# Performance work log

Measured on AMD Instinct MI355X. Metric: run time of the kernel, lower is better.

The kernel has to match this reference:

```python
import jax, jax.numpy as jnp
import numpy as np

D_MODEL = 1024
NHEAD = 16
HEAD_DIM = D_MODEL // NHEAD
DIM_FF = 4096
B, TC, TP = 4, 1024, 1024
EPS = 1e-5


def _layernorm(x, g, b):
    mu = jnp.mean(x, axis=-1, keepdims=True)
    var = jnp.mean(jnp.square(x - mu), axis=-1, keepdims=True)
    return (x - mu) * jax.lax.rsqrt(var + EPS) * g + b


def setup_inputs() -> dict:
    key = jax.random.key(0)
    ks = jax.random.split(key, 12)
    s = 0.02
    return {
        "x": jax.random.normal(ks[0], (B, TC, D_MODEL), jnp.float32),
        "Kp": jax.random.normal(ks[1], (B, NHEAD, TP, HEAD_DIM), jnp.float32),
        "Vp": jax.random.normal(ks[2], (B, NHEAD, TP, HEAD_DIM), jnp.float32),
        "pos_offset": TP,
        "wqkv": jax.random.normal(ks[3], (D_MODEL, 3 * D_MODEL), jnp.float32) * s,
        "bqkv": jnp.zeros((3 * D_MODEL,), jnp.float32),
        "wo": jax.random.normal(ks[4], (D_MODEL, D_MODEL), jnp.float32) * s,
        "bo": jnp.zeros((D_MODEL,), jnp.float32),
        "g1": jnp.ones((D_MODEL,), jnp.float32),
        "be1": jnp.zeros((D_MODEL,), jnp.float32),
        "g2": jnp.ones((D_MODEL,), jnp.float32),
        "be2": jnp.zeros((D_MODEL,), jnp.float32),
        "w1": jax.random.normal(ks[5], (D_MODEL, DIM_FF), jnp.float32) * s,
        "bf1": jnp.zeros((DIM_FF,), jnp.float32),
        "w2": jax.random.normal(ks[6], (DIM_FF, D_MODEL), jnp.float32) * s,
        "bf2": jnp.zeros((D_MODEL,), jnp.float32),
    }


def reference(x, Kp, Vp, pos_offset, wqkv, bqkv, wo, bo, g1, be1, g2, be2, w1, bf1, w2, bf2):
    Bsz, Tc, D = x.shape
    H, Dh = NHEAD, HEAD_DIM
    h = _layernorm(x, g1, be1)
    qkv = (h @ wqkv + bqkv).reshape(Bsz, Tc, 3, H, Dh).transpose(2, 0, 3, 1, 4)
    q, k_new, v_new = qkv[0], qkv[1], qkv[2]  # [B,H,Tc,Dh]
    K = jnp.concatenate([Kp, k_new], axis=2)  # [B,H,Tk,Dh]
    V = jnp.concatenate([Vp, v_new], axis=2)
    Tk = K.shape[2]
    scale = Dh ** -0.5
    # fused causal-masked attention; equivalent to the per-token loop:
    # query i attends keys j with j <= pos_offset + i
    scores = jnp.einsum("bhqd,bhkd->bhqk", q, K) * scale
    q_idx = jnp.arange(Tc)[:, None]
    k_idx = jnp.arange(Tk)[None, :]
    mask = k_idx <= (pos_offset + q_idx)  # [Tc,Tk]
    scores = jnp.where(mask, scores, jnp.finfo(scores.dtype).min)
    attn = jax.nn.softmax(scores, axis=-1)
    o = jnp.einsum("bhqk,bhkd->bhqd", attn, V)
    o = o.transpose(0, 2, 1, 3).reshape(Bsz, Tc, D)
    x = x + o @ wo + bo
    h2 = _layernorm(x, g2, be2)
    ff = jax.nn.gelu(h2 @ w1 + bf1, approximate=False) @ w2 + bf2
    x = x + ff
    return x, K, V
```

## Files before the change

### kernel.cpp

```cpp
#include <hip/hip_runtime.h>
#include <math.h>

#define DM   1024
#define NH   16
#define DH   64
#define DFF  4096
#define BSZ  4
#define TCC  1024
#define TPP  1024
#define TKK  2048
#define NTOK (BSZ*TCC)

typedef __attribute__((ext_vector_type(8))) short bf16x8;
typedef __attribute__((ext_vector_type(4))) float f32x4;

__device__ __forceinline__ unsigned short f2bf(float x) {
  union { float f; unsigned u; } v; v.f = x;
  unsigned r = v.u + 0x7fffu + ((v.u >> 16) & 1u);
  return (unsigned short)(r >> 16);
}
__device__ __forceinline__ unsigned pk2(float a, float b) {
  return (unsigned)f2bf(a) | ((unsigned)f2bf(b) << 16);
}

__device__ __forceinline__ void gload16(const void* g, void* l) {
  __builtin_amdgcn_global_load_lds(
      (const __attribute__((address_space(1))) void*)g,
      (__attribute__((address_space(3))) void*)l, 16, 0, 0);
}

__device__ __forceinline__ float wave_reduce_sum(float v) {
#pragma unroll
  for (int off = 32; off > 0; off >>= 1)
    v += __shfl_down(v, off, 64);
  return v;
}

__device__ __forceinline__ float gelu_f(float x) {
  float z = fabsf(x) * 0.70710678118654752440f;
  float t = 1.0f / (1.0f + 0.3275911f * z);
  float y = t * (0.254829592f +
            t * (-0.284496736f +
            t * (1.421413741f +
            t * (-1.453152027f +
            t * 1.061405429f))));
  float e = __expf(-z * z);
  float erfz = 1.0f - y * e;
  float s = (x >= 0.0f) ? erfz : -erfz;
  return 0.5f * x * (1.0f + s);
}

__global__ __launch_bounds__(256) void castT_kernel(
    const float* __restrict__ W, unsigned short* __restrict__ Wt, int K, int N) {
  __shared__ float tile[32][33];
  int nb = blockIdx.x << 5, kb = blockIdx.y << 5;
  int c = threadIdx.x & 31, r8 = threadIdx.x >> 5;
#pragma unroll
  for (int i = 0; i < 32; i += 8)
    tile[r8 + i][c] = W[(size_t)(kb + r8 + i) * N + nb + c];
  __syncthreads();
#pragma unroll
  for (int i = 0; i < 32; i += 8)
    Wt[(size_t)(nb + r8 + i) * K + kb + c] = f2bf(tile[c][r8 + i]);
}

__global__ __launch_bounds__(256) void castVt_kernel(
    const float* __restrict__ V, unsigned short* __restrict__ Vt) {
  __shared__ float tile[32][33];
  int z = blockIdx.z;
  const float* W = V + (size_t)z * TKK * DH;
  unsigned short* Wt = Vt + (size_t)z * DH * TKK;
  int nb = blockIdx.x << 5;
  int kb = blockIdx.y << 5;
  int c = threadIdx.x & 31, r8 = threadIdx.x >> 5;
#pragma unroll
  for (int i = 0; i < 32; i += 8)
    tile[r8 + i][c] = W[(size_t)(kb + r8 + i) * DH + nb + c];
  __syncthreads();
#pragma unroll
  for (int i = 0; i < 32; i += 8)
    Wt[(size_t)(nb + r8 + i) * TKK + kb + c] = f2bf(tile[c][r8 + i]);
}

__global__ __launch_bounds__(256) void copy_kv_kernel(
    const float4* __restrict__ Kp, const float4* __restrict__ Vp,
    float4* __restrict__ Kout, float4* __restrict__ Vout,
    unsigned short* __restrict__ Kbf) {
  int idx = blockIdx.x * 256 + threadIdx.x;
  int r = idx >> 4;
  int c = idx & 15;
  int dr = (r >> 10) * TKK + (r & 1023);
  float4 kv = Kp[idx];
  Kout[dr * 16 + c] = kv;
  Vout[dr * 16 + c] = Vp[idx];
  if (Kbf != nullptr) {
    uint2 pk;
    pk.x = pk2(kv.x, kv.y);
    pk.y = pk2(kv.z, kv.w);
    *(uint2*)(Kbf + (size_t)(dr * 16 + c) * 4) = pk;
  }
}

__global__ __launch_bounds__(256) void ln_kernel(
    const float* __restrict__ x, const float* __restrict__ g,
    const float* __restrict__ b, unsigned short* __restrict__ out) {
  __shared__ float red[8];
  int row = blockIdx.x;
  int tid = threadIdx.x;
  const float4* xr = (const float4*)(x + (size_t)row * DM);
  float4 xv = xr[tid];
  float s  = xv.x + xv.y + xv.z + xv.w;
  float ss = xv.x*xv.x + xv.y*xv.y + xv.z*xv.z + xv.w*xv.w;
  s  = wave_reduce_sum(s);
  ss = wave_reduce_sum(ss);
  int lane = tid & 63, wid = tid >> 6;
  if (lane == 0) { red[wid] = s; red[4 + wid] = ss; }
  __syncthreads();
  s  = red[0] + red[1] + red[2] + red[3];
  ss = red[4] + red[5] + red[6] + red[7];
  float mu  = s * (1.0f / DM);
  float var = ss * (1.0f / DM) - mu * mu;
  float rs  = rsqrtf(var + 1e-5f);
  float4 gv = ((const float4*)g)[tid];
  float4 bv = ((const float4*)b)[tid];
  ushort4 ov;
  ov.x = f2bf((xv.x - mu) * rs * gv.x + bv.x);
  ov.y = f2bf((xv.y - mu) * rs * gv.y + bv.y);
  ov.z = f2bf((xv.z - mu) * rs * gv.z + bv.z);
  ov.w = f2bf((xv.w - mu) * rs * gv.w + bv.w);
  *(ushort4*)&out[(size_t)row * DM + tid * 4] = ov;
}

template <int MODE, int NSPLIT>
__global__ __launch_bounds__(512) void mm8_kernel(
    const unsigned short* __restrict__ A, const unsigned short* __restrict__ Bt,
    const float* __restrict__ bias, const float* __restrict__ res,
    float* __restrict__ outf, unsigned short* __restrict__ outb,
    float* __restrict__ Kc, float* __restrict__ Vc,
    unsigned short* __restrict__ Kbfp,
    int M, int N, int K) {
  __shared__ __align__(16) short lds[4][2][8192];
  int tid = threadIdx.x;
  int l = tid & 63, w = tid >> 6;
  int wr = w >> 2, wc = w & 3;
  int cidx = l & 15, rg = l >> 4;
  int m0 = blockIdx.y << 8, n0 = blockIdx.x << 8;
  int z = (NSPLIT > 1) ? blockIdx.z : 0;
  int KS = K / NSPLIT;

  int r0 = tid >> 2;
  int cb = (((tid & 3) ^ ((r0 >> 1) & 3)) << 4);
  const char* gA = (const char*)A + (size_t)(m0 + r0) * 2 * K + cb + (size_t)2 * z * KS;
  const char* gB = (const char*)Bt + (size_t)(n0 + r0) * 2 * K + cb + (size_t)2 * z * KS;
  size_t rskip = (size_t)128 * 2 * K;

  int xcs = ((rg ^ ((cidx >> 1) & 3)) << 4);
  int offA = (wr * 128 + cidx) * 64 + xcs;
  int offB = (wc * 64 + cidx) * 64 + xcs;

  f32x4 acc[8][4] = {};
  int NT = KS >> 5;

  auto stage = [&](int t, int half) {
    char* la = (char*)&lds[t & 3][0][0] + tid * 16 + half * 8192;
    char* lb = (char*)&lds[t & 3][1][0] + tid * 16 + half * 8192;
    const char* sa = gA + t * 64 + (half ? rskip : 0);
    const char* sb = gB + t * 64 + (half ? rskip : 0);
    gload16(sa, la);
    gload16(sb, lb);
  };

  stage(0, 0); stage(0, 1);
  stage(1, 0); stage(1, 1);
  stage(2, 0); stage(2, 1);
  asm volatile("s_waitcnt vmcnt(8)" ::: "memory");
  __builtin_amdgcn_sched_barrier(0);
  __builtin_amdgcn_s_barrier();

  for (int t = 0; t < NT; ++t) {
    const char* pa = (const char*)&lds[t & 3][0][0];
    const char* pb = (const char*)&lds[t & 3][1][0];
    bf16x8 af[4], bg[4], a2[4];
#pragma unroll
    for (int i = 0; i < 4; ++i)
      af[i] = *(const bf16x8*)(pa + offA + i * 1024);
#pragma unroll
    for (int j = 0; j < 4; ++j)
      bg[j] = *(const bf16x8*)(pb + offB + j * 1024);
    if (t + 3 < NT) stage(t + 3, 0);
    __builtin_amdgcn_s_barrier();
    asm volatile("s_waitcnt lgkmcnt(0)" ::: "memory");
    __builtin_amdgcn_sched_barrier(0);
    __builtin_amdgcn_s_setprio(1);
#pragma unroll
    for (int i = 0; i < 4; ++i)
#pragma unroll
      for (int j = 0; j < 4; ++j)
        acc[i][j] = __builtin_amdgcn_mfma_f32_16x16x32_bf16(
            af[i], bg[j], acc[i][j], 0, 0, 0);
    __builtin_amdgcn_s_setprio(0);
    __builtin_amdgcn_s_barrier();
#pragma unroll
    for (int i = 0; i < 4; ++i)
      a2[i] = *(const bf16x8*)(pa + offA + (i + 4) * 1024);
    if (t + 3 < NT) stage(t + 3, 1);
    if (t + 3 < NT) {
      asm volatile("s_waitcnt vmcnt(8)" ::: "memory");
    } else if (t + 2 < NT) {
      asm volatile("s_waitcnt vmcnt(4)" ::: "memory");
    } else {
      asm volatile("s_waitcnt vmcnt(0)" ::: "memory");
    }
    __builtin_amdgcn_sched_barrier(0);
    __builtin_amdgcn_s_barrier();
    asm volatile("s_waitcnt lgkmcnt(0)" ::: "memory");
    __builtin_amdgcn_sched_barrier(0);
    __builtin_amdgcn_s_setprio(1);
#pragma unroll
    for (int i = 0; i < 4; ++i)
#pragma unroll
      for (int j = 0; j < 4; ++j)
        acc[i + 4][j] = __builtin_amdgcn_mfma_f32_16x16x32_bf16(
            a2[i], bg[j], acc[i + 4][j], 0, 0, 0);
    __builtin_amdgcn_s_setprio(0);
    __builtin_amdgcn_s_barrier();
  }

#pragma unroll
  for (int i = 0; i < 8; ++i) {
#pragma unroll
    for (int j = 0; j < 4; ++j) {
      int col = n0 + wc * 64 + j * 16 + cidx;
      float bb = bias[col];
#pragma unroll
      for (int r = 0; r < 4; ++r) {
        int row = m0 + wr * 128 + i * 16 + rg * 4 + r;
        float v = acc[i][j][r] + bb;
        if (MODE == 0) {
          int which = col >> 10, c = col & 1023;
          int hh = c >> 6, dd = c & 63;
          int b = row >> 10, tt = row & 1023;
          size_t base = (size_t)(b * NH + hh);
          if (which == 0)      outb[(base * TCC + tt) * DH + dd] = f2bf(v * 0.125f);
          else if (which == 1) {
            size_t off = (base * TKK + TPP + tt) * DH + dd;
            Kc[off] = v;
            if (Kbfp != nullptr) Kbfp[off] = f2bf(v);
          } else               Vc[(base * TKK + TPP + tt) * DH + dd] = v;
        } else if (MODE == 2) {
          outb[(size_t)row * N + col] = f2bf(gelu_f(v));
        } else {
          size_t off = (size_t)row * N + col;
          float add = acc[i][j][r];
          if (z == 0) add += bb + res[off];
          unsafeAtomicAdd(&outf[off], add);
        }
      }
    }
  }
}

template <int MODE, int DEPTH>
__global__ __launch_bounds__(256) void mm_kernel(
    const unsigned short* __restrict__ A, const unsigned short* __restrict__ Bt,
    const float* __restrict__ bias, const float* __restrict__ res,
    float* __restrict__ outf, unsigned short* __restrict__ outb,
    int M, int N, int K) {
  __shared__ __align__(16) short As[DEPTH * 128 * 32];
  __shared__ __align__(16) short Bs[DEPTH * 128 * 32];
  int tid = threadIdx.x;
  int w = tid >> 6, l = tid & 63;
  int m0 = blockIdx.y << 7, n0 = blockIdx.x << 7;
  int wm = (w >> 1) << 6, wn = (w & 1) << 6;
  int cidx = l & 15, rg = l >> 4;
  f32x4 acc[4][4] = {};

  int idx0 = w * 1024 + l * 16;
  int idx1 = idx0 + 4096;
  const char* gA0 = (const char*)A + (size_t)(m0 + (idx0 >> 6)) * 2 * K + (idx0 & 63);
  const char* gA1 = (const char*)A + (size_t)(m0 + (idx1 >> 6)) * 2 * K + (idx1 & 63);
  const char* gB0 = (const char*)Bt + (size_t)(n0 + (idx0 >> 6)) * 2 * K + (idx0 & 63);
  const char* gB1 = (const char*)Bt + (size_t)(n0 + (idx1 >> 6)) * 2 * K + (idx1 & 63);

  auto stage = [&](int bsel) {
    char* base_a = (char*)As + bsel * 8192;
    char* base_b = (char*)Bs + bsel * 8192;
    gload16(gA0, base_a + idx0); gload16(gA1, base_a + idx1);
    gload16(gB0, base_b + idx0); gload16(gB1, base_b + idx1);
    gA0 += 64; gA1 += 64; gB0 += 64; gB1 += 64;
  };
  auto compute = [&](int bsel) {
    const short* pa = As + bsel * 4096;
    const short* pb = Bs + bsel * 4096;
    bf16x8 af[4], bfr[4];
#pragma unroll
    for (int i = 0; i < 4; ++i) {
      af[i]  = *(const bf16x8*)&pa[(wm + i * 16 + cidx) * 32 + rg * 8];
      bfr[i] = *(const bf16x8*)&pb[(wn + i * 16 + cidx) * 32 + rg * 8];
    }
#pragma unroll
    for (int i = 0; i < 4; ++i)
#pragma unroll
      for (int j = 0; j < 4; ++j)
        acc[i][j] = __builtin_amdgcn_mfma_f32_16x16x32_bf16(
            af[i], bfr[j], acc[i][j], 0, 0, 0);
  };

  int nt = K >> 5;
  stage(0); stage(1); stage(2);
  for (int t = 0; t < nt - 3; ++t) {
    asm volatile("s_waitcnt vmcnt(8)" ::: "memory");
    __builtin_amdgcn_sched_barrier(0);
    __builtin_amdgcn_s_barrier();
    __builtin_amdgcn_sched_barrier(0);
    stage((t + 3) & 3);
    compute(t & 3);
  }
  asm volatile("s_waitcnt vmcnt(8)" ::: "memory");
  __builtin_amdgcn_sched_barrier(0);
  __builtin_amdgcn_s_barrier();
  __builtin_amdgcn_sched_barrier(0);
  compute((nt - 3) & 3);
  asm volatile("s_waitcnt vmcnt(4)" ::: "memory");
  __builtin_amdgcn_sched_barrier(0);
  __builtin_amdgcn_s_barrier();
  __builtin_amdgcn_sched_barrier(0);
  compute((nt - 2) & 3);
  asm volatile("s_waitcnt vmcnt(0)" ::: "memory");
  __builtin_amdgcn_sched_barrier(0);
  __builtin_amdgcn_s_barrier();
  __builtin_amdgcn_sched_barrier(0);
  compute((nt - 1) & 3);

#pragma unroll
  for (int i = 0; i < 4; ++i) {
#pragma unroll
    for (int j = 0; j < 4; ++j) {
      int col = n0 + wn + j * 16 + cidx;
      float bb = bias[col];
#pragma unroll
      for (int r = 0; r < 4; ++r) {
        int row = m0 + wm + i * 16 + rg * 4 + r;
        float v = acc[i][j][r] + bb;
        size_t off = (size_t)row * N + col;
        outf[off] = res[off] + v;
      }
    }
  }
}

template <int KBF>
__global__ __launch_bounds__(256) void attn_kernel(
    const unsigned short* __restrict__ Qb, const float* __restrict__ K,
    const unsigned short* __restrict__ Kb16,
    const unsigned short* __restrict__ Vtb, const int* __restrict__ posp,
    unsigned short* __restrict__ o) {
  __shared__ __align__(16) unsigned short Qs[64][72];
  __shared__ __align__(16) unsigned short Ks[64][72];
  __shared__ __align__(16) unsigned short Vts[64][72];
  __shared__ __align__(16) unsigned short Pw[4][16][72];
  int tid = threadIdx.x;
  int w = tid >> 6, lane = tid & 63;
  int l15 = lane & 15, quad = lane >> 4;
  int blk = blockIdx.x;
  int bh = blk >> 4;
  int qbase = (blk & 15) << 6;
  int b = bh >> 4, h = bh & 15;
  int pos = *posp;

  {
    int r = tid >> 2, cg = (tid & 3) << 4;
    const unsigned short* src = Qb + ((size_t)bh * TCC + qbase + r) * DH + cg;
    *(uint4*)&Qs[r][cg]     = *(const uint4*)src;
    *(uint4*)&Qs[r][cg + 8] = *(const uint4*)(src + 8);
  }
  __syncthreads();
  bf16x8 aq0 = *(const bf16x8*)&Qs[16 * w + l15][quad * 8];
  bf16x8 aq1 = *(const bf16x8*)&Qs[16 * w + l15][32 + quad * 8];

  f32x4 accO[4] = {};
  f32x4 accL = {};
  bf16x8 ones;
#pragma unroll
  for (int i = 0; i < 8; ++i) ones[i] = (short)0x3F80;

  int nk = pos + qbase + 64; if (nk > TKK) nk = TKK;
  int ntiles = nk >> 6;
  const float* Kbh = K + (size_t)bh * TKK * DH;
  const unsigned short* Kbh16 = Kb16 + (size_t)bh * TKK * DH;
  const unsigned short* Vbh = Vtb + (size_t)bh * DH * TKK;

  for (int t = 0; t < ntiles; ++t) {
    int kt = t << 6;
    {
      int r = tid >> 2, cg = (tid & 3) << 4;
      if (KBF) {
        const unsigned short* ks = Kbh16 + (size_t)(kt + r) * DH + cg;
        *(uint4*)&Ks[r][cg]     = *(const uint4*)ks;
        *(uint4*)&Ks[r][cg + 8] = *(const uint4*)(ks + 8);
      } else {
        const float* ks = Kbh + (size_t)(kt + r) * DH + cg;
        float4 k0 = *(const float4*)ks,       k1 = *(const float4*)(ks + 4);
        float4 k2 = *(const float4*)(ks + 8), k3 = *(const float4*)(ks + 12);
        uint4 p0, p1;
        p0.x = pk2(k0.x, k0.y); p0.y = pk2(k0.z, k0.w);
        p0.z = pk2(k1.x, k1.y); p0.w = pk2(k1.z, k1.w);
        p1.x = pk2(k2.x, k2.y); p1.y = pk2(k2.z, k2.w);
        p1.z = pk2(k3.x, k3.y); p1.w = pk2(k3.z, k3.w);
        *(uint4*)&Ks[r][cg]     = p0;
        *(uint4*)&Ks[r][cg + 8] = p1;
      }
      const unsigned short* vs = Vbh + (size_t)r * TKK + kt + cg;
      *(uint4*)&Vts[r][cg]     = *(const uint4*)vs;
      *(uint4*)&Vts[r][cg + 8] = *(const uint4*)(vs + 8);
    }
    __syncthreads();
    f32x4 accS[4] = {};
    __builtin_amdgcn_s_setprio(1);
#pragma unroll
    for (int j = 0; j < 4; ++j) {
      bf16x8 bk0 = *(const bf16x8*)&Ks[16 * j + l15][quad * 8];
      bf16x8 bk1 = *(const bf16x8*)&Ks[16 * j + l15][32 + quad * 8];
      accS[j] = __builtin_amdgcn_mfma_f32_16x16x32_bf16(aq0, bk0, accS[j], 0, 0, 0);
      accS[j] = __builtin_amdgcn_mfma_f32_16x16x32_bf16(aq1, bk1, accS[j], 0, 0, 0);
    }
    __builtin_amdgcn_s_setprio(0);
    bool edge = (kt + 63 > pos + qbase);
#pragma unroll
    for (int j = 0; j < 4; ++j) {
      int key = kt + 16 * j + l15;
#pragma unroll
      for (int r = 0; r < 4; ++r) {
        float p = __expf(accS[j][r]);
        if (edge && key > pos + qbase + 16 * w + quad * 4 + r) p = 0.f;
        Pw[w][quad * 4 + r][16 * j + l15] = f2bf(p);
      }
    }
    bf16x8 ap0 = *(const bf16x8*)&Pw[w][l15][quad * 8];
    bf16x8 ap1 = *(const bf16x8*)&Pw[w][l15][32 + quad * 8];
    __builtin_amdgcn_s_setprio(1);
    accL = __builtin_amdgcn_mfma_f32_16x16x32_bf16(ap0, ones, accL, 0, 0, 0);
    accL = __builtin_amdgcn_mfma_f32_16x16x32_bf16(ap1, ones, accL, 0, 0, 0);
#pragma unroll
    for (int j2 = 0; j2 < 4; ++j2) {
      bf16x8 bv0 = *(const bf16x8*)&Vts[16 * j2 + l15][quad * 8];
      bf16x8 bv1 = *(const bf16x8*)&Vts[16 * j2 + l15][32 + quad * 8];
      accO[j2] = __builtin_amdgcn_mfma_f32_16x16x32_bf16(ap0, bv0, accO[j2], 0, 0, 0);
      accO[j2] = __builtin_amdgcn_mfma_f32_16x16x32_bf16(ap1, bv1, accO[j2], 0, 0, 0);
    }
    __builtin_amdgcn_s_setprio(0);
    __syncthreads();
  }
#pragma unroll
  for (int r = 0; r < 4; ++r) {
    float inv = 1.0f / accL[r];
    int qg = qbase + 16 * w + quad * 4 + r;
    size_t base = (((size_t)(b * TCC + qg)) * NH + h) * DH;
#pragma unroll
    for (int j2 = 0; j2 < 4; ++j2)
      o[base + 16 * j2 + l15] = f2bf(accO[j2][r] * inv);
  }
}

extern "C" void kernel_launch(void* const* d_in, const int* in_sizes, int n_in,
                              void* d_out, int out_size, void* d_ws, size_t ws_size,
                              hipStream_t stream) {
  (void)in_sizes; (void)n_in; (void)out_size;
  const float* x    = (const float*)d_in[0];
  const float* Kp   = (const float*)d_in[1];
  const float* Vp   = (const float*)d_in[2];
  const int*   posp = (const int*)d_in[3];
  const float* wqkv = (const float*)d_in[4];
  const float* bqkv = (const float*)d_in[5];
  const float* wo   = (const float*)d_in[6];
  const float* bo   = (const float*)d_in[7];
  const float* g1   = (const float*)d_in[8];
  const float* be1  = (const float*)d_in[9];
  const float* g2   = (const float*)d_in[10];
  const float* be2  = (const float*)d_in[11];
  const float* w1   = (const float*)d_in[12];
  const float* bf1  = (const float*)d_in[13];
  const float* w2   = (const float*)d_in[14];
  const float* bf2  = (const float*)d_in[15];

  float* xout = (float*)d_out;
  float* Kout = xout + (size_t)BSZ * TCC * DM;
  float* Vout = Kout + (size_t)BSZ * NH * TKK * DH;

  const size_t MB = 1024 * 1024;
  char* ws = (char*)d_ws;
  unsigned short* wqkvT = (unsigned short*)(ws);
  unsigned short* woT   = (unsigned short*)(ws + 6 * MB);
  unsigned short* w1T   = (unsigned short*)(ws + 8 * MB);
  unsigned short* w2T   = (unsigned short*)(ws + 16 * MB);
  unsigned short* hbf   = (unsigned short*)(ws + 24 * MB);
  unsigned short* ffbf  = (unsigned short*)(ws + 32 * MB);
  unsigned short* Qbuf  = (unsigned short*)(ws + 32 * MB);
  unsigned short* obf   = (unsigned short*)(ws + 40 * MB);
  unsigned short* Vtb   = (unsigned short*)(ws + 48 * MB);
  unsigned short* Kbf   = (ws_size >= 80 * MB)
                            ? (unsigned short*)(ws + 64 * MB) : nullptr;
  bool big = (ws_size >= 96 * MB);
  float* x2 = big ? (float*)(ws + 80 * MB) : xout;

  if (big) {
    hipMemsetAsync(x2,   0, (size_t)NTOK * DM * sizeof(float), stream);
    hipMemsetAsync(xout, 0, (size_t)NTOK * DM * sizeof(float), stream);
  }

  castT_kernel<<<dim3(96, 32),  dim3(256), 0, stream>>>(wqkv, wqkvT, DM, 3 * DM);
  castT_kernel<<<dim3(32, 32),  dim3(256), 0, stream>>>(wo,   woT,   DM, DM);
  castT_kernel<<<dim3(128, 32), dim3(256), 0, stream>>>(w1,   w1T,   DM, DFF);
  castT_kernel<<<dim3(32, 128), dim3(256), 0, stream>>>(w2,   w2T,   DFF, DM);

  copy_kv_kernel<<<dim3(4096), dim3(256), 0, stream>>>(
      (const float4*)Kp, (const float4*)Vp, (float4*)Kout, (float4*)Vout, Kbf);
  ln_kernel<<<dim3(NTOK), dim3(256), 0, stream>>>(x, g1, be1, hbf);
  mm8_kernel<0, 1><<<dim3(12, 16), dim3(512), 0, stream>>>(
      hbf, wqkvT, bqkv, nullptr, nullptr, Qbuf, Kout, Vout, Kbf, NTOK, 3 * DM, DM);
  castVt_kernel<<<dim3(2, 64, 64), dim3(256), 0, stream>>>(Vout, Vtb);
  if (Kbf != nullptr)
    attn_kernel<1><<<dim3(1024), dim3(256), 0, stream>>>(Qbuf, Kout, Kbf, Vtb, posp, obf);
  else
    attn_kernel<0><<<dim3(1024), dim3(256), 0, stream>>>(Qbuf, Kout, Kbf, Vtb, posp, obf);

  if (big) {
    mm8_kernel<3, 4><<<dim3(4, 16, 4), dim3(512), 0, stream>>>(
        obf, woT, bo, x, x2, nullptr, nullptr, nullptr, nullptr, NTOK, DM, DM);
    ln_kernel<<<dim3(NTOK), dim3(256), 0, stream>>>(x2, g2, be2, hbf);
    mm8_kernel<2, 1><<<dim3(16, 16), dim3(512), 0, stream>>>(
        hbf, w1T, bf1, nullptr, nullptr, ffbf, nullptr, nullptr, nullptr, NTOK, DFF, DM);
    mm8_kernel<3, 4><<<dim3(4, 16, 4), dim3(512), 0, stream>>>(
        ffbf, w2T, bf2, x2, xout, nullptr, nullptr, nullptr, nullptr, NTOK, DM, DFF);
  } else {
    mm_kernel<1, 4><<<dim3(8, 32), dim3(256), 0, stream>>>(
        obf, woT, bo, x, x2, nullptr, NTOK, DM, DM);
    ln_kernel<<<dim3(NTOK), dim3(256), 0, stream>>>(x2, g2, be2, hbf);
    mm8_kernel<2, 1><<<dim3(16, 16), dim3(512), 0, stream>>>(
        hbf, w1T, bf1, nullptr, nullptr, ffbf, nullptr, nullptr, nullptr, NTOK, DFF, DM);
    mm_kernel<1, 4><<<dim3(8, 32), dim3(256), 0, stream>>>(
        ffbf, w2T, bf2, x2, xout, nullptr, NTOK, DM, DFF);
  }
}
```

Measured before the change: 584.1 us.

## Replace atomic split-K output projections with plain partial stores plus reduction kernel

The out-projection now always uses the non-split mm_kernel, so its atomic split-K path and the two memsets are gone. The FF2 GEMM uses a 2-way split-K that writes plain stores into two workspace partial buffers, and a new elementwise kernel adds both partials, the bias and the residual into the output. This removes atomic contention and the zero-fill traffic, at the cost of an extra launch and a read/write pass over two 16MB partial buffers. pfA aliases the transposed-weight region at ws offset 0 and pfB aliases the Kbf region, which reuses buffers that are no longer needed at that point.

```diff
diff --git a/kernel.cpp b/kernel.cpp
--- a/kernel.cpp
+++ b/kernel.cpp
@@ -131,6 +131,21 @@
   *(ushort4*)&out[(size_t)row * DM + tid * 4] = ov;
 }
 
+__global__ __launch_bounds__(256) void reduce2_kernel(
+    float* __restrict__ xout, const float* __restrict__ bf2,
+    const float* __restrict__ pA, const float* __restrict__ pB) {
+  int idx = blockIdx.x * 256 + threadIdx.x;
+  float4 o = ((const float4*)xout)[idx];
+  float4 b = ((const float4*)bf2)[idx & 255];
+  float4 a = ((const float4*)pA)[idx];
+  float4 c = ((const float4*)pB)[idx];
+  o.x += b.x + a.x + c.x;
+  o.y += b.y + a.y + c.y;
+  o.z += b.z + a.z + c.z;
+  o.w += b.w + a.w + c.w;
+  ((float4*)xout)[idx] = o;
+}
+
 template <int MODE, int NSPLIT>
 __global__ __launch_bounds__(512) void mm8_kernel(
     const unsigned short* __restrict__ A, const unsigned short* __restrict__ Bt,
@@ -250,10 +265,8 @@
         } else if (MODE == 2) {
           outb[(size_t)row * N + col] = f2bf(gelu_f(v));
         } else {
-          size_t off = (size_t)row * N + col;
-          float add = acc[i][j][r];
-          if (z == 0) add += bb + res[off];
-          unsafeAtomicAdd(&outf[off], add);
+          float* dst = (z == 0) ? outf : Kc;
+          dst[(size_t)row * N + col] = acc[i][j][r];
         }
       }
     }
@@ -498,15 +511,11 @@
   unsigned short* Qbuf  = (unsigned short*)(ws + 32 * MB);
   unsigned short* obf   = (unsigned short*)(ws + 40 * MB);
   unsigned short* Vtb   = (unsigned short*)(ws + 48 * MB);
-  unsigned short* Kbf   = (ws_size >= 80 * MB)
-                            ? (unsigned short*)(ws + 64 * MB) : nullptr;
-  bool big = (ws_size >= 96 * MB);
-  float* x2 = big ? (float*)(ws + 80 * MB) : xout;
-
-  if (big) {
-    hipMemsetAsync(x2,   0, (size_t)NTOK * DM * sizeof(float), stream);
-    hipMemsetAsync(xout, 0, (size_t)NTOK * DM * sizeof(float), stream);
-  }
+  float*          x2    = xout;
+  bool big = (ws_size >= 80 * MB);
+  unsigned short* Kbf = big ? (unsigned short*)(ws + 64 * MB) : nullptr;
+  float* pfA = (float*)(ws);
+  float* pfB = (float*)(ws + 64 * MB);
 
   castT_kernel<<<dim3(96, 32),  dim3(256), 0, stream>>>(wqkv, wqkvT, DM, 3 * DM);
   castT_kernel<<<dim3(32, 32),  dim3(256), 0, stream>>>(wo,   woT,   DM, DM);
@@ -523,22 +532,17 @@
     attn_kernel<1><<<dim3(1024), dim3(256), 0, stream>>>(Qbuf, Kout, Kbf, Vtb, posp, obf);
   else
     attn_kernel<0><<<dim3(1024), dim3(256), 0, stream>>>(Qbuf, Kout, Kbf, Vtb, posp, obf);
-
+  mm_kernel<1, 4><<<dim3(8, 32), dim3(256), 0, stream>>>(
+      obf, woT, bo, x, x2, nullptr, NTOK, DM, DM);
+  ln_kernel<<<dim3(NTOK), dim3(256), 0, stream>>>(x2, g2, be2, hbf);
+  mm8_kernel<2, 1><<<dim3(16, 16), dim3(512), 0, stream>>>(
+      hbf, w1T, bf1, nullptr, nullptr, ffbf, nullptr, nullptr, nullptr, NTOK, DFF, DM);
   if (big) {
-    mm8_kernel<3, 4><<<dim3(4, 16, 4), dim3(512), 0, stream>>>(
-        obf, woT, bo, x, x2, nullptr, nullptr, nullptr, nullptr, NTOK, DM, DM);
-    ln_kernel<<<dim3(NTOK), dim3(256), 0, stream>>>(x2, g2, be2, hbf);
-    mm8_kernel<2, 1><<<dim3(16, 16), dim3(512), 0, stream>>>(
-        hbf, w1T, bf1, nullptr, nullptr, ffbf, nullptr, nullptr, nullptr, NTOK, DFF, DM);
-    mm8_kernel<3, 4><<<dim3(4, 16, 4), dim3(512), 0, stream>>>(
-        ffbf, w2T, bf2, x2, xout, nullptr, nullptr, nullptr, nullptr, NTOK, DM, DFF);
+    mm8_kernel<4, 2><<<dim3(4, 16, 2), dim3(512), 0, stream>>>(
+        ffbf, w2T, bf2, nullptr, pfA, nullptr, pfB, nullptr, nullptr, NTOK, DM, DFF);
+    reduce2_kernel<<<dim3(4096), dim3(256), 0, stream>>>(xout, bf2, pfA, pfB);
   } else {
     mm_kernel<1, 4><<<dim3(8, 32), dim3(256), 0, stream>>>(
-        obf, woT, bo, x, x2, nullptr, NTOK, DM, DM);
-    ln_kernel<<<dim3(NTOK), dim3(256), 0, stream>>>(x2, g2, be2, hbf);
-    mm8_kernel<2, 1><<<dim3(16, 16), dim3(512), 0, stream>>>(
-        hbf, w1T, bf1, nullptr, nullptr, ffbf, nullptr, nullptr, nullptr, NTOK, DFF, DM);
-    mm_kernel<1, 4><<<dim3(8, 32), dim3(256), 0, stream>>>(
         ffbf, w2T, bf2, x2, xout, nullptr, NTOK, DM, DFF);
   }
 }
```

Result: faster. 471.3 us (-19.3%).
